# Kernel tuning notes

Hardware: AMD Instinct MI355X
Metric: run time of the kernel (lower is better)

Reference implementation:

```python
import jax, jax.numpy as jnp
import numpy as np

B, K, U, V, D = 4096, 32, 32768, 100000, 128


def setup_inputs() -> dict:
    key = jax.random.key(0)
    k1, k2, k3 = jax.random.split(key, 3)
    neigh_cols = jax.random.randint(k1, (B, K), 0, U, dtype=jnp.int32)
    unique_ids = jax.random.randint(k2, (U,), 0, V, dtype=jnp.int32)
    embed_table = jax.random.normal(k3, (V, D), dtype=jnp.float32)
    return {"neigh_cols": neigh_cols, "unique_ids": unique_ids, "embed_table": embed_table}


def reference(neigh_cols, unique_ids, embed_table):
    # Build dense binary neighbor mask [B, U]; duplicate (row, col) pairs
    # collapse to 1.0, matching the original set semantics.
    rows = jnp.arange(B, dtype=jnp.int32)[:, None]          # [B, 1]
    mask = jnp.zeros((B, U), jnp.float32).at[rows, neigh_cols].set(1.0)
    # Symmetric sqrt-degree normalization (row then column).
    row_norm = jnp.sqrt(mask.sum(axis=1, keepdims=True))    # [B, 1], always >= 1
    col_norm = jnp.sqrt(mask.sum(axis=0, keepdims=True))    # [1, U]
    # Guard columns that no row touches (original would produce NaN there,
    # but those columns are all-zero so the guarded result is identical where defined).
    mask = mask / row_norm / jnp.maximum(col_norm, 1.0)
    # Gather embeddings of the unique nodes, then sparse-as-dense matmul.
    embed_matrix = embed_table[unique_ids]                  # [U, D]
    to_feats = mask @ embed_matrix                          # [B, D]
    return to_feats
```

## Files before the change

kernel.cpp:

```cpp
#include <hip/hip_runtime.h>

#define B_ROWS 4096
#define KNZ 32
#define U_COLS 32768
#define D_DIM 128
#define ROWS_PER_BLOCK 8

__global__ __launch_bounds__(256) void col_deg_kernel(
    const int* __restrict__ neigh, int* __restrict__ col_deg)
{
    int b = blockIdx.x * blockDim.x + threadIdx.x;
    if (b >= B_ROWS) return;
    int c[KNZ];
#pragma unroll
    for (int k = 0; k < KNZ; ++k) c[k] = neigh[b * KNZ + k];
#pragma unroll
    for (int k = 0; k < KNZ; ++k) {
        bool dup = false;
#pragma unroll
        for (int j = 0; j < KNZ; ++j) {
            if (j < k) dup = dup || (c[j] == c[k]);
        }
        if (!dup) atomicAdd(&col_deg[c[k]], 1);
    }
}

__global__ __launch_bounds__(256) void aggregate_kernel(
    const int* __restrict__ neigh, const int* __restrict__ uids,
    const float* __restrict__ embed, const int* __restrict__ col_deg,
    float* __restrict__ out)
{
    __shared__ int   s_cols[ROWS_PER_BLOCK][KNZ];
    __shared__ int   s_eidx[ROWS_PER_BLOCK][KNZ];
    __shared__ float s_w[ROWS_PER_BLOCK][KNZ];
    __shared__ float s_rs[ROWS_PER_BLOCK];

    const int r    = threadIdx.x >> 5;
    const int lane = threadIdx.x & 31;
    const int b    = blockIdx.x * ROWS_PER_BLOCK + r;

    const int c = neigh[b * KNZ + lane];
    s_cols[r][lane] = c;
    __syncthreads();

    bool keep = true;
    for (int j = 0; j < lane; ++j) keep = keep && (s_cols[r][j] != c);

    unsigned long long bm = __ballot(keep);
    unsigned int half = (threadIdx.x & 32) ? (unsigned int)(bm >> 32)
                                           : (unsigned int)(bm & 0xffffffffULL);
    int row_deg = __popc(half);

    s_w[r][lane]    = keep ? rsqrtf((float)col_deg[c]) : 0.0f;
    s_eidx[r][lane] = uids[c];
    if (lane == 0) s_rs[r] = rsqrtf((float)row_deg);
    __syncthreads();

    const float4* ev = (const float4*)embed;
    float4 acc = make_float4(0.f, 0.f, 0.f, 0.f);
#pragma unroll 8
    for (int j = 0; j < KNZ; ++j) {
        const float w = s_w[r][j];
        const long long idx = (long long)s_eidx[r][j] * (D_DIM / 4) + lane;
        const float4 e = ev[idx];
        acc.x += w * e.x;
        acc.y += w * e.y;
        acc.z += w * e.z;
        acc.w += w * e.w;
    }
    const float rs = s_rs[r];
    float4 o = make_float4(acc.x * rs, acc.y * rs, acc.z * rs, acc.w * rs);
    ((float4*)out)[(long long)b * (D_DIM / 4) + lane] = o;
}

extern "C" void kernel_launch(void* const* d_in, const int* in_sizes, int n_in,
                              void* d_out, int out_size, void* d_ws, size_t ws_size,
                              hipStream_t stream) {
    const int*   neigh = (const int*)d_in[0];
    const int*   uids  = (const int*)d_in[1];
    const float* embed = (const float*)d_in[2];
    float*       out   = (float*)d_out;
    int*         col_deg = (int*)d_ws;

    hipMemsetAsync(col_deg, 0, U_COLS * sizeof(int), stream);

    col_deg_kernel<<<B_ROWS / 256, 256, 0, stream>>>(neigh, col_deg);

    aggregate_kernel<<<B_ROWS / ROWS_PER_BLOCK, 256, 0, stream>>>(
        neigh, uids, embed, col_deg, out);
}
```

Measured before the change: 111.1 us.

## Fuse memset, column-degree and aggregation into one cooperative kernel with grid syncs

Replaces the memset plus two kernel launches with a single cooperative kernel. It zeroes the column degrees, counts them atomically and aggregates embeddings, with two grid-wide barriers separating the phases. It also reuses the per-row duplicate check for the degree count and moves the uid lookup earlier. The aim is to remove launch and inter-kernel gaps, at the cost of grid sync overhead and a requirement that all 512 blocks be co-resident.

```diff
diff --git a/kernel.cpp b/kernel.cpp
--- a/kernel.cpp
+++ b/kernel.cpp
@@ -1,35 +1,22 @@
 #include <hip/hip_runtime.h>
+#include <hip/hip_cooperative_groups.h>
+
+namespace cg = cooperative_groups;
 
 #define B_ROWS 4096
 #define KNZ 32
 #define U_COLS 32768
 #define D_DIM 128
 #define ROWS_PER_BLOCK 8
+#define NBLOCKS (B_ROWS / ROWS_PER_BLOCK)
 
-__global__ __launch_bounds__(256) void col_deg_kernel(
-    const int* __restrict__ neigh, int* __restrict__ col_deg)
-{
-    int b = blockIdx.x * blockDim.x + threadIdx.x;
-    if (b >= B_ROWS) return;
-    int c[KNZ];
-#pragma unroll
-    for (int k = 0; k < KNZ; ++k) c[k] = neigh[b * KNZ + k];
-#pragma unroll
-    for (int k = 0; k < KNZ; ++k) {
-        bool dup = false;
-#pragma unroll
-        for (int j = 0; j < KNZ; ++j) {
-            if (j < k) dup = dup || (c[j] == c[k]);
-        }
-        if (!dup) atomicAdd(&col_deg[c[k]], 1);
-    }
-}
-
-__global__ __launch_bounds__(256) void aggregate_kernel(
+__global__ __launch_bounds__(256, 2) void gcn_fused_kernel(
     const int* __restrict__ neigh, const int* __restrict__ uids,
-    const float* __restrict__ embed, const int* __restrict__ col_deg,
+    const float* __restrict__ embed, int* __restrict__ col_deg,
     float* __restrict__ out)
 {
+    cg::grid_group grid = cg::this_grid();
+
     __shared__ int   s_cols[ROWS_PER_BLOCK][KNZ];
     __shared__ int   s_eidx[ROWS_PER_BLOCK][KNZ];
     __shared__ float s_w[ROWS_PER_BLOCK][KNZ];
@@ -38,9 +25,13 @@
     const int r    = threadIdx.x >> 5;
     const int lane = threadIdx.x & 31;
     const int b    = blockIdx.x * ROWS_PER_BLOCK + r;
+    const int tid  = blockIdx.x * blockDim.x + threadIdx.x;
+
+    if (tid < U_COLS) col_deg[tid] = 0;
 
     const int c = neigh[b * KNZ + lane];
     s_cols[r][lane] = c;
+    s_eidx[r][lane] = uids[c];
     __syncthreads();
 
     bool keep = true;
@@ -49,11 +40,16 @@
     unsigned long long bm = __ballot(keep);
     unsigned int half = (threadIdx.x & 32) ? (unsigned int)(bm >> 32)
                                            : (unsigned int)(bm & 0xffffffffULL);
-    int row_deg = __popc(half);
+    const int row_deg = __popc(half);
+    if (lane == 0) s_rs[r] = rsqrtf((float)row_deg);
 
-    s_w[r][lane]    = keep ? rsqrtf((float)col_deg[c]) : 0.0f;
-    s_eidx[r][lane] = uids[c];
-    if (lane == 0) s_rs[r] = rsqrtf((float)row_deg);
+    grid.sync();
+
+    if (keep) atomicAdd(&col_deg[c], 1);
+
+    grid.sync();
+
+    s_w[r][lane] = keep ? rsqrtf((float)col_deg[c]) : 0.0f;
     __syncthreads();
 
     const float4* ev = (const float4*)embed;
@@ -76,16 +72,14 @@
 extern "C" void kernel_launch(void* const* d_in, const int* in_sizes, int n_in,
                               void* d_out, int out_size, void* d_ws, size_t ws_size,
                               hipStream_t stream) {
-    const int*   neigh = (const int*)d_in[0];
-    const int*   uids  = (const int*)d_in[1];
-    const float* embed = (const float*)d_in[2];
-    float*       out   = (float*)d_out;
+    const int*   neigh   = (const int*)d_in[0];
+    const int*   uids    = (const int*)d_in[1];
+    const float* embed   = (const float*)d_in[2];
+    float*       out     = (float*)d_out;
     int*         col_deg = (int*)d_ws;
 
-    hipMemsetAsync(col_deg, 0, U_COLS * sizeof(int), stream);
-
-    col_deg_kernel<<<B_ROWS / 256, 256, 0, stream>>>(neigh, col_deg);
-
-    aggregate_kernel<<<B_ROWS / ROWS_PER_BLOCK, 256, 0, stream>>>(
-        neigh, uids, embed, col_deg, out);
+    void* args[] = {(void*)&neigh, (void*)&uids, (void*)&embed,
+                    (void*)&col_deg, (void*)&out};
+    hipLaunchCooperativeKernel((void*)gcn_fused_kernel,
+                               dim3(NBLOCKS), dim3(256), args, 0, stream);
 }
```

New measurement: 202.9 us. +82.7%, slower.
